# Kernel optimization log

Measured on AMD Instinct MI355X. Metric: run time of the kernel, lower is better.

Reference implementation:

```python
import jax, jax.numpy as jnp
import numpy as np

B, S, D = 32, 4096, 512   # batch, seq_len, input_dim
A, K = 3, 4               # attractor_dim, num_attractors
OUT = 512                 # output_dim


def setup_inputs() -> dict:
    key = jax.random.key(0)
    ks = jax.random.split(key, 10)
    s = 0.02
    return {
        "x": jax.random.normal(ks[0], (B, S, D), dtype=jnp.float32),
        "centers": jax.random.normal(ks[1], (K, A), dtype=jnp.float32),
        "Wa": jax.random.normal(ks[2], (D, A), dtype=jnp.float32) * s,
        "ba": jnp.zeros((A,), dtype=jnp.float32),
        "Wh": jax.random.normal(ks[3], (A, 2 * A), dtype=jnp.float32) * 0.5,
        "bh": jnp.zeros((2 * A,), dtype=jnp.float32),
        "Wk": jax.random.normal(ks[4], (2 * A, K), dtype=jnp.float32) * 0.5,
        "bk": jnp.zeros((K,), dtype=jnp.float32),
        "Wout": jax.random.normal(ks[5], (K * D, OUT), dtype=jnp.float32) * s,
        "bout": jnp.zeros((OUT,), dtype=jnp.float32),
    }


def reference(x, centers, Wa, ba, Wh, bh, Wk, bk, Wout, bout):
    # project to attractor space: [B,S,A]
    af = jnp.einsum("bsd,da->bsa", x, Wa) + ba
    # L2 distance to each attractor center: [B,S,K]
    diff = af[:, :, :, None] - centers.T[None, None, :, :]   # [B,S,A,K]
    distances = jnp.sqrt(jnp.sum(diff * diff, axis=2))
    # tiny MLP weights (batched over all timesteps at once): [B,S,K]
    base = jax.nn.relu(af @ Wh + bh) @ Wk + bk
    distance_weights = jax.nn.softmax(-distances, axis=-1)
    final_weights = jax.nn.softmax(base + distance_weights, axis=-1)
    # attractor-weighted pooling over time, concatenated attractor-major: [B, K*D]
    pooled = jnp.einsum("bsk,bsd->bkd", final_weights, x).reshape(x.shape[0], -1)
    return pooled @ Wout + bout
```

## Files before the change

kernel.cpp:

```cpp
#include <hip/hip_runtime.h>
#include <cstdint>
#include <cstddef>

#define BB 32
#define SS 4096
#define DD 512
#define AA 3
#define KK 4
#define OUTD 512

#define NCH 32
#define ROWS_PER_BLOCK (SS / NCH)
#define TR 16
#define NIT (ROWS_PER_BLOCK / TR)
#define XROW 520

__device__ __forceinline__ void load_tile(const float* __restrict__ xb,
                                          int s0, int tid, float4 st[8]) {
    #pragma unroll
    for (int t = 0; t < 8; ++t) {
        const int idx = tid + t * 256;
        const int row = idx >> 7;
        const int c4  = (idx & 127) << 2;
        st[t] = *(const float4*)(xb + (size_t)(s0 + row) * DD + c4);
    }
}

__global__ __launch_bounds__(256) void fused_pool_kernel(
    const float* __restrict__ x, const float* __restrict__ centers,
    const float* __restrict__ Wa, const float* __restrict__ ba,
    const float* __restrict__ Wh, const float* __restrict__ bh,
    const float* __restrict__ Wk, const float* __restrict__ bk,
    float* __restrict__ partial)
{
    __shared__ alignas(16) float  xs[TR * XROW];
    __shared__ alignas(16) float  wat[AA * DD];
    __shared__ float  sw[68];
    __shared__ float4 fw_sh[TR];

    const int tid   = threadIdx.x;
    const int b     = blockIdx.y;
    const int chunk = blockIdx.x;

    if (tid < 12)      sw[tid] = centers[tid];
    else if (tid < 15) sw[tid] = ba[tid - 12];
    else if (tid < 33) sw[tid] = Wh[tid - 15];
    else if (tid < 39) sw[tid] = bh[tid - 33];
    else if (tid < 63) sw[tid] = Wk[tid - 39];
    else if (tid < 67) sw[tid] = bk[tid - 63];
    for (int d = tid; d < DD; d += 256) {
        wat[0 * DD + d] = Wa[d * 3 + 0];
        wat[1 * DD + d] = Wa[d * 3 + 1];
        wat[2 * DD + d] = Wa[d * 3 + 2];
    }

    const int g    = tid >> 4;
    const int l16  = tid & 15;
    const int half = tid >> 7;
    const int c4   = (tid & 127) << 2;
    const int s_base = chunk * ROWS_PER_BLOCK;
    const float* xb = x + (size_t)b * SS * DD;

    float4 acc0 = {0,0,0,0}, acc1 = {0,0,0,0}, acc2 = {0,0,0,0}, acc3 = {0,0,0,0};

    float4 stA[8], stB[8];
    load_tile(xb, s_base, tid, stA);

    auto step = [&](float4 (&cur)[8], float4 (&nxt)[8], int it) {
        #pragma unroll
        for (int t = 0; t < 8; ++t)
            *(float4*)(xs + (half + 2 * t) * XROW + c4) = cur[t];
        if (it + 1 < NIT)
            load_tile(xb, s_base + (it + 1) * TR, tid, nxt);
        __syncthreads();

        {
            const float* xrow = xs + g * XROW;
            float p0 = 0.f, p1 = 0.f, p2 = 0.f;
            #pragma unroll
            for (int i = 0; i < 8; ++i) {
                const int c = l16 * 4 + i * 64;
                float4 v  = *(const float4*)(xrow + c);
                float4 w0 = *(const float4*)(wat + c);
                float4 w1 = *(const float4*)(wat + DD + c);
                float4 w2 = *(const float4*)(wat + 2 * DD + c);
                p0 += v.x * w0.x + v.y * w0.y + v.z * w0.z + v.w * w0.w;
                p1 += v.x * w1.x + v.y * w1.y + v.z * w1.z + v.w * w1.w;
                p2 += v.x * w2.x + v.y * w2.y + v.z * w2.z + v.w * w2.w;
            }
            #pragma unroll
            for (int off = 8; off >= 1; off >>= 1) {
                p0 += __shfl_xor(p0, off);
                p1 += __shfl_xor(p1, off);
                p2 += __shfl_xor(p2, off);
            }
            const float af0 = p0 + sw[12];
            const float af1 = p1 + sw[13];
            const float af2 = p2 + sw[14];

            float dist[KK];
            #pragma unroll
            for (int k = 0; k < KK; ++k) {
                float da = af0 - sw[k * 3 + 0];
                float db = af1 - sw[k * 3 + 1];
                float dc = af2 - sw[k * 3 + 2];
                dist[k] = sqrtf(da * da + db * db + dc * dc);
            }
            float mn = fminf(fminf(dist[0], dist[1]), fminf(dist[2], dist[3]));
            float e[KK]; float esum = 0.f;
            #pragma unroll
            for (int k = 0; k < KK; ++k) { e[k] = __expf(mn - dist[k]); esum += e[k]; }
            const float einv = 1.0f / esum;

            float h[6];
            #pragma unroll
            for (int i6 = 0; i6 < 6; ++i6) {
                float v = af0 * sw[15 + i6] + af1 * sw[21 + i6]
                        + af2 * sw[27 + i6] + sw[33 + i6];
                h[i6] = fmaxf(v, 0.0f);
            }
            float logit[KK];
            #pragma unroll
            for (int k = 0; k < KK; ++k) {
                float v = sw[63 + k];
                #pragma unroll
                for (int i6 = 0; i6 < 6; ++i6) v += h[i6] * sw[39 + i6 * 4 + k];
                logit[k] = v + e[k] * einv;
            }
            float mx = fmaxf(fmaxf(logit[0], logit[1]), fmaxf(logit[2], logit[3]));
            float f0 = __expf(logit[0] - mx), f1 = __expf(logit[1] - mx);
            float f2 = __expf(logit[2] - mx), f3 = __expf(logit[3] - mx);
            const float finv = 1.0f / (f0 + f1 + f2 + f3);
            if (l16 == 0)
                fw_sh[g] = make_float4(f0 * finv, f1 * finv, f2 * finv, f3 * finv);
        }
        __syncthreads();

        #pragma unroll
        for (int t = 0; t < 8; ++t) {
            float4 v = cur[t];
            float4 f = fw_sh[half + 2 * t];
            acc0.x += f.x * v.x; acc0.y += f.x * v.y; acc0.z += f.x * v.z; acc0.w += f.x * v.w;
            acc1.x += f.y * v.x; acc1.y += f.y * v.y; acc1.z += f.y * v.z; acc1.w += f.y * v.w;
            acc2.x += f.z * v.x; acc2.y += f.z * v.y; acc2.z += f.z * v.z; acc2.w += f.z * v.w;
            acc3.x += f.w * v.x; acc3.y += f.w * v.y; acc3.z += f.w * v.z; acc3.w += f.w * v.w;
        }
    };

    #pragma unroll 1
    for (int it = 0; it < NIT; it += 2) {
        step(stA, stB, it);
        step(stB, stA, it + 1);
    }

    __syncthreads();
    float4* red = (float4*)xs;
    if (half == 1) {
        red[(tid - 128) * 4 + 0] = acc0;
        red[(tid - 128) * 4 + 1] = acc1;
        red[(tid - 128) * 4 + 2] = acc2;
        red[(tid - 128) * 4 + 3] = acc3;
    }
    __syncthreads();
    if (half == 0) {
        float4 o0 = red[tid * 4 + 0], o1 = red[tid * 4 + 1];
        float4 o2 = red[tid * 4 + 2], o3 = red[tid * 4 + 3];
        acc0.x += o0.x; acc0.y += o0.y; acc0.z += o0.z; acc0.w += o0.w;
        acc1.x += o1.x; acc1.y += o1.y; acc1.z += o1.z; acc1.w += o1.w;
        acc2.x += o2.x; acc2.y += o2.y; acc2.z += o2.z; acc2.w += o2.w;
        acc3.x += o3.x; acc3.y += o3.y; acc3.z += o3.z; acc3.w += o3.w;
        float* pp = partial + ((size_t)b * NCH + chunk) * (KK * DD);
        *(float4*)(pp + 0 * DD + c4) = acc0;
        *(float4*)(pp + 1 * DD + c4) = acc1;
        *(float4*)(pp + 2 * DD + c4) = acc2;
        *(float4*)(pp + 3 * DD + c4) = acc3;
    }
}

__global__ __launch_bounds__(256) void out_gemm_kernel(
    const float* __restrict__ partial, const float* __restrict__ Wout,
    const float* __restrict__ bout, float* __restrict__ out)
{
    __shared__ float  p_sh[2048];
    __shared__ float4 red4[8][32];
    const int tid = threadIdx.x;
    const int cc = blockIdx.x, b = blockIdx.y;

    {
        const float4* pbase = (const float4*)(partial + (size_t)b * NCH * 2048);
        #pragma unroll
        for (int s = 0; s < 2; ++s) {
            const int slot = tid + s * 256;
            float4 a = {0,0,0,0};
            #pragma unroll 4
            for (int c = 0; c < NCH; ++c) {
                float4 v = pbase[(size_t)c * 512 + slot];
                a.x += v.x; a.y += v.y; a.z += v.z; a.w += v.w;
            }
            *(float4*)(p_sh + slot * 4) = a;
        }
    }
    __syncthreads();

    const int q  = tid & 31;
    const int js = tid >> 5;
    const int colbase = cc * 128 + q * 4;
    const float* wp = Wout + (size_t)(js * 256) * OUTD + colbase;
    float4 a = {0,0,0,0};
    #pragma unroll 8
    for (int j = 0; j < 256; ++j) {
        float4 w = *(const float4*)(wp + (size_t)j * OUTD);
        float  p = p_sh[js * 256 + j];
        a.x += p * w.x; a.y += p * w.y; a.z += p * w.z; a.w += p * w.w;
    }
    red4[js][q] = a;
    __syncthreads();

    if (tid < 128) {
        const int qq = tid >> 2, e = tid & 3;
        float s = 0.f;
        #pragma unroll
        for (int s8 = 0; s8 < 8; ++s8)
            s += ((const float*)&red4[s8][qq])[e];
        const int col = cc * 128 + tid;
        out[b * OUTD + col] = s + bout[col];
    }
}

extern "C" void kernel_launch(void* const* d_in, const int* in_sizes, int n_in,
                              void* d_out, int out_size, void* d_ws, size_t ws_size,
                              hipStream_t stream) {
    (void)in_sizes; (void)n_in; (void)out_size; (void)ws_size;
    const float* x       = (const float*)d_in[0];
    const float* centers = (const float*)d_in[1];
    const float* Wa      = (const float*)d_in[2];
    const float* ba      = (const float*)d_in[3];
    const float* Wh      = (const float*)d_in[4];
    const float* bh      = (const float*)d_in[5];
    const float* Wk      = (const float*)d_in[6];
    const float* bk      = (const float*)d_in[7];
    const float* Wout    = (const float*)d_in[8];
    const float* bout    = (const float*)d_in[9];
    float* out     = (float*)d_out;
    float* partial = (float*)d_ws;

    fused_pool_kernel<<<dim3(NCH, BB), 256, 0, stream>>>(
        x, centers, Wa, ba, Wh, bh, Wk, bk, partial);
    out_gemm_kernel<<<dim3(4, BB), 256, 0, stream>>>(partial, Wout, bout, out);
}
```

Before: 413.6 us.

## Process rows per-wavefront in registers, removing LDS staging and block barriers

Measured after the change: 422.3 us. 1.02x slower.

```diff
diff --git a/kernel.cpp b/kernel.cpp
--- a/kernel.cpp
+++ b/kernel.cpp
@@ -10,20 +10,18 @@
 #define OUTD 512
 
 #define NCH 32
-#define ROWS_PER_BLOCK (SS / NCH)
-#define TR 16
-#define NIT (ROWS_PER_BLOCK / TR)
-#define XROW 520
-
-__device__ __forceinline__ void load_tile(const float* __restrict__ xb,
-                                          int s0, int tid, float4 st[8]) {
-    #pragma unroll
-    for (int t = 0; t < 8; ++t) {
-        const int idx = tid + t * 256;
-        const int row = idx >> 7;
-        const int c4  = (idx & 127) << 2;
-        st[t] = *(const float4*)(xb + (size_t)(s0 + row) * DD + c4);
-    }
+#define RPB (SS / NCH)
+#define RPW 32
+#define NIT (RPW / 2)
+
+__device__ __forceinline__ float rfl(float x) {
+    return __uint_as_float(__builtin_amdgcn_readfirstlane(__float_as_uint(x)));
+}
+__device__ __forceinline__ float dot4(const float4& a, const float4& b) {
+    return a.x * b.x + a.y * b.y + a.z * b.z + a.w * b.w;
+}
+__device__ __forceinline__ void fma4(float4& a, float s, const float4& v) {
+    a.x += s * v.x; a.y += s * v.y; a.z += s * v.z; a.w += s * v.w;
 }
 
 __global__ __launch_bounds__(256) void fused_pool_kernel(
@@ -33,147 +31,152 @@
     const float* __restrict__ Wk, const float* __restrict__ bk,
     float* __restrict__ partial)
 {
-    __shared__ alignas(16) float  xs[TR * XROW];
-    __shared__ alignas(16) float  wat[AA * DD];
-    __shared__ float  sw[68];
-    __shared__ float4 fw_sh[TR];
-
-    const int tid   = threadIdx.x;
-    const int b     = blockIdx.y;
-    const int chunk = blockIdx.x;
-
-    if (tid < 12)      sw[tid] = centers[tid];
-    else if (tid < 15) sw[tid] = ba[tid - 12];
-    else if (tid < 33) sw[tid] = Wh[tid - 15];
-    else if (tid < 39) sw[tid] = bh[tid - 33];
-    else if (tid < 63) sw[tid] = Wk[tid - 39];
-    else if (tid < 67) sw[tid] = bk[tid - 63];
+    __shared__ float shmem[4 * 2048];
+
+    const int tid = threadIdx.x;
+    const int w   = tid >> 6;
+    const int l   = tid & 63;
+    const int b = blockIdx.y, chunk = blockIdx.x;
+
+    float ctr[12], bav[3], whv[18], bhv[6], wkv[24], bkv[4];
+    #pragma unroll
+    for (int i = 0; i < 12; ++i) ctr[i] = rfl(centers[i]);
+    #pragma unroll
+    for (int i = 0; i < 3; ++i)  bav[i] = rfl(ba[i]);
+    #pragma unroll
+    for (int i = 0; i < 18; ++i) whv[i] = rfl(Wh[i]);
+    #pragma unroll
+    for (int i = 0; i < 6; ++i)  bhv[i] = rfl(bh[i]);
+    #pragma unroll
+    for (int i = 0; i < 24; ++i) wkv[i] = rfl(Wk[i]);
+    #pragma unroll
+    for (int i = 0; i < 4; ++i)  bkv[i] = rfl(bk[i]);
+
     for (int d = tid; d < DD; d += 256) {
-        wat[0 * DD + d] = Wa[d * 3 + 0];
-        wat[1 * DD + d] = Wa[d * 3 + 1];
-        wat[2 * DD + d] = Wa[d * 3 + 2];
-    }
-
-    const int g    = tid >> 4;
-    const int l16  = tid & 15;
-    const int half = tid >> 7;
-    const int c4   = (tid & 127) << 2;
-    const int s_base = chunk * ROWS_PER_BLOCK;
-    const float* xb = x + (size_t)b * SS * DD;
-
-    float4 acc0 = {0,0,0,0}, acc1 = {0,0,0,0}, acc2 = {0,0,0,0}, acc3 = {0,0,0,0};
-
-    float4 stA[8], stB[8];
-    load_tile(xb, s_base, tid, stA);
-
-    auto step = [&](float4 (&cur)[8], float4 (&nxt)[8], int it) {
-        #pragma unroll
-        for (int t = 0; t < 8; ++t)
-            *(float4*)(xs + (half + 2 * t) * XROW + c4) = cur[t];
-        if (it + 1 < NIT)
-            load_tile(xb, s_base + (it + 1) * TR, tid, nxt);
-        __syncthreads();
-
-        {
-            const float* xrow = xs + g * XROW;
-            float p0 = 0.f, p1 = 0.f, p2 = 0.f;
+        shmem[0 * DD + d] = Wa[d * 3 + 0];
+        shmem[1 * DD + d] = Wa[d * 3 + 1];
+        shmem[2 * DD + d] = Wa[d * 3 + 2];
+    }
+    __syncthreads();
+    const int c0 = l * 4;
+    float4 wa[3][2];
+    #pragma unroll
+    for (int a = 0; a < 3; ++a) {
+        wa[a][0] = *(const float4*)&shmem[a * DD + c0];
+        wa[a][1] = *(const float4*)&shmem[a * DD + c0 + 256];
+    }
+
+    const int s0 = chunk * RPB + w * RPW;
+    const float* xr = x + (size_t)b * SS * DD + (size_t)s0 * DD + c0;
+
+    float4 acc[KK][2];
+    #pragma unroll
+    for (int k = 0; k < KK; ++k)
+        #pragma unroll
+        for (int h = 0; h < 2; ++h)
+            acc[k][h] = make_float4(0.f, 0.f, 0.f, 0.f);
+
+    auto load4 = [&](int it, float4 st[4]) {
+        const float* p = xr + (size_t)it * (2 * DD);
+        st[0] = *(const float4*)(p);
+        st[1] = *(const float4*)(p + 256);
+        st[2] = *(const float4*)(p + DD);
+        st[3] = *(const float4*)(p + DD + 256);
+    };
+
+    auto rowfw = [&](float af0, float af1, float af2) -> float4 {
+        float dist[KK];
+        #pragma unroll
+        for (int k = 0; k < KK; ++k) {
+            float da = af0 - ctr[k * 3 + 0];
+            float db = af1 - ctr[k * 3 + 1];
+            float dc = af2 - ctr[k * 3 + 2];
+            dist[k] = sqrtf(da * da + db * db + dc * dc);
+        }
+        float mn = fminf(fminf(dist[0], dist[1]), fminf(dist[2], dist[3]));
+        float e[KK]; float esum = 0.f;
+        #pragma unroll
+        for (int k = 0; k < KK; ++k) { e[k] = __expf(mn - dist[k]); esum += e[k]; }
+        const float einv = 1.0f / esum;
+
+        float h6[6];
+        #pragma unroll
+        for (int i = 0; i < 6; ++i) {
+            float v = af0 * whv[i] + af1 * whv[6 + i] + af2 * whv[12 + i] + bhv[i];
+            h6[i] = fmaxf(v, 0.0f);
+        }
+        float logit[KK];
+        #pragma unroll
+        for (int k = 0; k < KK; ++k) {
+            float v = bkv[k];
             #pragma unroll
-            for (int i = 0; i < 8; ++i) {
-                const int c = l16 * 4 + i * 64;
-                float4 v  = *(const float4*)(xrow + c);
-                float4 w0 = *(const float4*)(wat + c);
-                float4 w1 = *(const float4*)(wat + DD + c);
-                float4 w2 = *(const float4*)(wat + 2 * DD + c);
-                p0 += v.x * w0.x + v.y * w0.y + v.z * w0.z + v.w * w0.w;
-                p1 += v.x * w1.x + v.y * w1.y + v.z * w1.z + v.w * w1.w;
-                p2 += v.x * w2.x + v.y * w2.y + v.z * w2.z + v.w * w2.w;
-            }
-            #pragma unroll
-            for (int off = 8; off >= 1; off >>= 1) {
-                p0 += __shfl_xor(p0, off);
-                p1 += __shfl_xor(p1, off);
-                p2 += __shfl_xor(p2, off);
-            }
-            const float af0 = p0 + sw[12];
-            const float af1 = p1 + sw[13];
-            const float af2 = p2 + sw[14];
-
-            float dist[KK];
-            #pragma unroll
-            for (int k = 0; k < KK; ++k) {
-                float da = af0 - sw[k * 3 + 0];
-                float db = af1 - sw[k * 3 + 1];
-                float dc = af2 - sw[k * 3 + 2];
-                dist[k] = sqrtf(da * da + db * db + dc * dc);
-            }
-            float mn = fminf(fminf(dist[0], dist[1]), fminf(dist[2], dist[3]));
-            float e[KK]; float esum = 0.f;
-            #pragma unroll
-            for (int k = 0; k < KK; ++k) { e[k] = __expf(mn - dist[k]); esum += e[k]; }
-            const float einv = 1.0f / esum;
-
-            float h[6];
-            #pragma unroll
-            for (int i6 = 0; i6 < 6; ++i6) {
-                float v = af0 * sw[15 + i6] + af1 * sw[21 + i6]
-                        + af2 * sw[27 + i6] + sw[33 + i6];
-                h[i6] = fmaxf(v, 0.0f);
-            }
-            float logit[KK];
-            #pragma unroll
-            for (int k = 0; k < KK; ++k) {
-                float v = sw[63 + k];
-                #pragma unroll
-                for (int i6 = 0; i6 < 6; ++i6) v += h[i6] * sw[39 + i6 * 4 + k];
-                logit[k] = v + e[k] * einv;
-            }
-            float mx = fmaxf(fmaxf(logit[0], logit[1]), fmaxf(logit[2], logit[3]));
-            float f0 = __expf(logit[0] - mx), f1 = __expf(logit[1] - mx);
-            float f2 = __expf(logit[2] - mx), f3 = __expf(logit[3] - mx);
-            const float finv = 1.0f / (f0 + f1 + f2 + f3);
-            if (l16 == 0)
-                fw_sh[g] = make_float4(f0 * finv, f1 * finv, f2 * finv, f3 * finv);
-        }
-        __syncthreads();
-
-        #pragma unroll
-        for (int t = 0; t < 8; ++t) {
-            float4 v = cur[t];
-            float4 f = fw_sh[half + 2 * t];
-            acc0.x += f.x * v.x; acc0.y += f.x * v.y; acc0.z += f.x * v.z; acc0.w += f.x * v.w;
-            acc1.x += f.y * v.x; acc1.y += f.y * v.y; acc1.z += f.y * v.z; acc1.w += f.y * v.w;
-            acc2.x += f.z * v.x; acc2.y += f.z * v.y; acc2.z += f.z * v.z; acc2.w += f.z * v.w;
-            acc3.x += f.w * v.x; acc3.y += f.w * v.y; acc3.z += f.w * v.z; acc3.w += f.w * v.w;
-        }
+            for (int i = 0; i < 6; ++i) v += h6[i] * wkv[i * 4 + k];
+            logit[k] = v + e[k] * einv;
+        }
+        float mx = fmaxf(fmaxf(logit[0], logit[1]), fmaxf(logit[2], logit[3]));
+        float f0 = __expf(logit[0] - mx), f1 = __expf(logit[1] - mx);
+        float f2 = __expf(logit[2] - mx), f3 = __expf(logit[3] - mx);
+        const float finv = 1.0f / (f0 + f1 + f2 + f3);
+        return make_float4(f0 * finv, f1 * finv, f2 * finv, f3 * finv);
     };
 
+    auto body = [&](const float4 st[4]) {
+        float p00 = dot4(st[0], wa[0][0]) + dot4(st[1], wa[0][1]);
+        float p01 = dot4(st[0], wa[1][0]) + dot4(st[1], wa[1][1]);
+        float p02 = dot4(st[0], wa[2][0]) + dot4(st[1], wa[2][1]);
+        float p10 = dot4(st[2], wa[0][0]) + dot4(st[3], wa[0][1]);
+        float p11 = dot4(st[2], wa[1][0]) + dot4(st[3], wa[1][1]);
+        float p12 = dot4(st[2], wa[2][0]) + dot4(st[3], wa[2][1]);
+        #pragma unroll
+        for (int off = 32; off >= 1; off >>= 1) {
+            p00 += __shfl_xor(p00, off);
+            p01 += __shfl_xor(p01, off);
+            p02 += __shfl_xor(p02, off);
+            p10 += __shfl_xor(p10, off);
+            p11 += __shfl_xor(p11, off);
+            p12 += __shfl_xor(p12, off);
+        }
+        float4 f0 = rowfw(p00 + bav[0], p01 + bav[1], p02 + bav[2]);
+        float4 f1 = rowfw(p10 + bav[0], p11 + bav[1], p12 + bav[2]);
+        #pragma unroll
+        for (int h = 0; h < 2; ++h) {
+            fma4(acc[0][h], f0.x, st[h]); fma4(acc[1][h], f0.y, st[h]);
+            fma4(acc[2][h], f0.z, st[h]); fma4(acc[3][h], f0.w, st[h]);
+            fma4(acc[0][h], f1.x, st[2 + h]); fma4(acc[1][h], f1.y, st[2 + h]);
+            fma4(acc[2][h], f1.z, st[2 + h]); fma4(acc[3][h], f1.w, st[2 + h]);
+        }
+    };
+
+    float4 stA[4], stB[4];
+    load4(0, stA);
     #pragma unroll 1
     for (int it = 0; it < NIT; it += 2) {
-        step(stA, stB, it);
-        step(stB, stA, it + 1);
-    }
-
-    __syncthreads();
-    float4* red = (float4*)xs;
-    if (half == 1) {
-        red[(tid - 128) * 4 + 0] = acc0;
-        red[(tid - 128) * 4 + 1] = acc1;
-        red[(tid - 128) * 4 + 2] = acc2;
-        red[(tid - 128) * 4 + 3] = acc3;
-    }
-    __syncthreads();
-    if (half == 0) {
-        float4 o0 = red[tid * 4 + 0], o1 = red[tid * 4 + 1];
-        float4 o2 = red[tid * 4 + 2], o3 = red[tid * 4 + 3];
-        acc0.x += o0.x; acc0.y += o0.y; acc0.z += o0.z; acc0.w += o0.w;
-        acc1.x += o1.x; acc1.y += o1.y; acc1.z += o1.z; acc1.w += o1.w;
-        acc2.x += o2.x; acc2.y += o2.y; acc2.z += o2.z; acc2.w += o2.w;
-        acc3.x += o3.x; acc3.y += o3.y; acc3.z += o3.z; acc3.w += o3.w;
-        float* pp = partial + ((size_t)b * NCH + chunk) * (KK * DD);
-        *(float4*)(pp + 0 * DD + c4) = acc0;
-        *(float4*)(pp + 1 * DD + c4) = acc1;
-        *(float4*)(pp + 2 * DD + c4) = acc2;
-        *(float4*)(pp + 3 * DD + c4) = acc3;
+        if (it + 1 < NIT) load4(it + 1, stB);
+        body(stA);
+        if (it + 2 < NIT) load4(it + 2, stA);
+        body(stB);
+    }
+
+    __syncthreads();
+    #pragma unroll
+    for (int k = 0; k < KK; ++k)
+        #pragma unroll
+        for (int h = 0; h < 2; ++h)
+            *(float4*)&shmem[w * 2048 + k * 512 + h * 256 + c0] = acc[k][h];
+    __syncthreads();
+    float* pp = partial + ((size_t)b * NCH + chunk) * (KK * DD);
+    #pragma unroll
+    for (int s = 0; s < 2; ++s) {
+        const int off = (tid + s * 256) * 4;
+        float4 r0 = *(const float4*)&shmem[0 * 2048 + off];
+        float4 r1 = *(const float4*)&shmem[1 * 2048 + off];
+        float4 r2 = *(const float4*)&shmem[2 * 2048 + off];
+        float4 r3 = *(const float4*)&shmem[3 * 2048 + off];
+        float4 r = make_float4(r0.x + r1.x + r2.x + r3.x,
+                               r0.y + r1.y + r2.y + r3.y,
+                               r0.z + r1.z + r2.z + r3.z,
+                               r0.w + r1.w + r2.w + r3.w);
+        *(float4*)(pp + off) = r;
     }
 }
 
@@ -191,7 +194,7 @@
         #pragma unroll
         for (int s = 0; s < 2; ++s) {
             const int slot = tid + s * 256;
-            float4 a = {0,0,0,0};
+            float4 a = {0, 0, 0, 0};
             #pragma unroll 4
             for (int c = 0; c < NCH; ++c) {
                 float4 v = pbase[(size_t)c * 512 + slot];
@@ -206,12 +209,12 @@
     const int js = tid >> 5;
     const int colbase = cc * 128 + q * 4;
     const float* wp = Wout + (size_t)(js * 256) * OUTD + colbase;
-    float4 a = {0,0,0,0};
+    float4 a = {0, 0, 0, 0};
     #pragma unroll 8
     for (int j = 0; j < 256; ++j) {
-        float4 w = *(const float4*)(wp + (size_t)j * OUTD);
+        float4 wv = *(const float4*)(wp + (size_t)j * OUTD);
         float  p = p_sh[js * 256 + j];
-        a.x += p * w.x; a.y += p * w.y; a.z += p * w.z; a.w += p * w.w;
+        a.x += p * wv.x; a.y += p * wv.y; a.z += p * wv.z; a.w += p * wv.w;
     }
     red4[js][q] = a;
     __syncthreads();
```
